# Optimization experiments

Measured on AMD Instinct MI355X. Metric: run time of the kernel, lower is better.

Reference implementation:

```python
import jax, jax.numpy as jnp
import numpy as np

B, S, D = 16, 4096, 1024
K = 65536  # number of keys == number of concepts (identity mapping)
EPS = 1e-12


def setup_inputs() -> dict:
    key = jax.random.key(0)
    k1, k2, k3, k4, k5, k6 = jax.random.split(key, 6)
    return {
        "hidden": jax.random.normal(k1, (B, S, D), dtype=jnp.float32),
        "concept_signal": jax.random.normal(k2, (B, 1, D), dtype=jnp.float32),
        "keys": jax.random.normal(k3, (K, D), dtype=jnp.float32),
        "values": jax.random.normal(k4, (K, 1, D), dtype=jnp.float32),
        "key_to_value": jnp.arange(K, dtype=jnp.int64),
        "W_layer": jax.random.normal(k5, (D, D), dtype=jnp.float32) * 0.02,
        "b_layer": jax.random.normal(k6, (D,), dtype=jnp.float32) * 0.02,
    }


def _l2norm(x, axis=-1):
    return x / jnp.maximum(jnp.linalg.norm(x, axis=axis, keepdims=True), EPS)


def reference(hidden, concept_signal, keys, values, key_to_value, W_layer, b_layer):
    # self.layer(hidden_state): Linear(D, D)
    layer_out = jnp.einsum("bsd,ed->bse", hidden, W_layer) + b_layer  # [B, S, D]

    # Tensor branch of forward: per-sample nearest-key search.
    # q: one query position per sample (P=1) -> [B, D]
    q = concept_signal[:, 0, :]
    cos = jnp.einsum("bd,kd->bk", _l2norm(q), _l2norm(keys))  # cosine similarity [B, K]
    dist = 1.0 - cos                                           # cosine distance
    chosen_key = jnp.argmin(dist, axis=1)                      # [B] nearest key per sample
    # s = 1 - smallest_dist; with threshold=-2.0 it always passes; with
    # max_tokens_per_concept=1, k = max(1, ceil(clamp(s,0,1)*1)) == 1 token.
    concept_idx = key_to_value[chosen_key]                     # [B]
    tokens = values[concept_idx, 0, :]                         # [B, D] (first of the k=1 tokens)
    tokens = _l2norm(tokens)                                   # F.normalize(..., p=2, dim=-1)
    # vstack one token onto each sample, then stack -> [B, S+1, D]
    return jnp.concatenate([layer_out, tokens[:, None, :]], axis=1)
```

## Files before the change

kernel.cpp:

```cpp
#include <hip/hip_runtime.h>

constexpr int BB = 16;
constexpr int SS = 4096;
constexpr int DD = 1024;
constexpr int KK = 65536;
constexpr int GM = BB * SS;
constexpr int GK = DD;

typedef __attribute__((ext_vector_type(8))) short bf16x8;
typedef __attribute__((ext_vector_type(4))) float f32x4;
typedef __attribute__((ext_vector_type(8))) unsigned short ushort8;

#define GLD_LDS16(g, l)                                                        \
  __builtin_amdgcn_global_load_lds(                                            \
      (const __attribute__((address_space(1))) void*)(g),                      \
      (__attribute__((address_space(3))) void*)(l), 16, 0, 0)

__device__ __forceinline__ unsigned short f2bf(float x) {
  unsigned u = __float_as_uint(x);
  u += 0x7fffu + ((u >> 16) & 1u);
  return (unsigned short)(u >> 16);
}

__device__ __forceinline__ void cvt_body(const float* __restrict__ in,
                                         unsigned short* __restrict__ out,
                                         int i) {
  const float4* p = (const float4*)in + (size_t)i * 2;
  float4 a = p[0], b = p[1];
  ushort8 r;
  r[0] = f2bf(a.x); r[1] = f2bf(a.y); r[2] = f2bf(a.z); r[3] = f2bf(a.w);
  r[4] = f2bf(b.x); r[5] = f2bf(b.y); r[6] = f2bf(b.z); r[7] = f2bf(b.w);
  *(ushort8*)(out + (size_t)i * 8) = r;
}

__global__ __launch_bounds__(256) void qsplit(const float* __restrict__ csig,
                                              unsigned short* __restrict__ qh,
                                              unsigned short* __restrict__ ql) {
  int i = blockIdx.x * 256 + threadIdx.x;
  float v = csig[i];
  unsigned short h = f2bf(v);
  float hf = __uint_as_float((unsigned)h << 16);
  qh[i] = h;
  ql[i] = f2bf(v - hf);
}

__device__ __forceinline__ void cos_mfma_body(
    const float* __restrict__ keys, const unsigned short* __restrict__ qh,
    const unsigned short* __restrict__ ql, float* __restrict__ pscore,
    int* __restrict__ pidx, int cblk, int tid,
    float (*rs)[16], int (*ri)[16]) {
  int lane = tid & 63, w = tid >> 6;
  int fr = lane & 15, kg = lane >> 4;
  int key = cblk * 64 + w * 16 + fr;

  const float* krow = keys + (size_t)key * DD + kg * 8;
  const unsigned short* qhp = qh + fr * DD + kg * 8;
  const unsigned short* qlp = ql + fr * DD + kg * 8;

  f32x4 acc = {};
  float nrm = 0.f;

  float4 ka0, kb0, ka1, kb1, ka2, kb2, ka3, kb3;
  bf16x8 h0, l0, h1, l1, h2, l2, h3, l3;

  ka0 = *(const float4*)(krow);      kb0 = *(const float4*)(krow + 4);
  h0  = *(const bf16x8*)(qhp);       l0  = *(const bf16x8*)(qlp);
  ka1 = *(const float4*)(krow + 32); kb1 = *(const float4*)(krow + 36);
  h1  = *(const bf16x8*)(qhp + 32);  l1  = *(const bf16x8*)(qlp + 32);
  ka2 = *(const float4*)(krow + 64); kb2 = *(const float4*)(krow + 68);
  h2  = *(const bf16x8*)(qhp + 64);  l2  = *(const bf16x8*)(qlp + 64);

#define COS_STEP(KA, KB, HH, LL, KAP, KBP, HP, LP, T) do {                     \
    if ((T) + 3 < 32) {                                                        \
      KAP = *(const float4*)(krow + ((T) + 3) * 32);                           \
      KBP = *(const float4*)(krow + ((T) + 3) * 32 + 4);                       \
      HP  = *(const bf16x8*)(qhp + ((T) + 3) * 32);                            \
      LP  = *(const bf16x8*)(qlp + ((T) + 3) * 32);                            \
    }                                                                          \
    float ke[8] = {KA.x, KA.y, KA.z, KA.w, KB.x, KB.y, KB.z, KB.w};            \
    ushort8 khv, klv;                                                          \
    _Pragma("unroll") for (int j = 0; j < 8; ++j) {                            \
      float v = ke[j];                                                         \
      unsigned short h = f2bf(v);                                              \
      float hf = __uint_as_float((unsigned)h << 16);                           \
      khv[j] = h;                                                              \
      klv[j] = f2bf(v - hf);                                                   \
      nrm = fmaf(v, v, nrm);                                                   \
    }                                                                          \
    bf16x8 kh8 = *(bf16x8*)&khv, kl8 = *(bf16x8*)&klv;                         \
    acc = __builtin_amdgcn_mfma_f32_16x16x32_bf16(HH, kh8, acc, 0, 0, 0);      \
    acc = __builtin_amdgcn_mfma_f32_16x16x32_bf16(LL, kh8, acc, 0, 0, 0);      \
    acc = __builtin_amdgcn_mfma_f32_16x16x32_bf16(HH, kl8, acc, 0, 0, 0);      \
  } while (0)

#pragma unroll
  for (int tt = 0; tt < 32; tt += 4) {
    COS_STEP(ka0, kb0, h0, l0, ka3, kb3, h3, l3, tt + 0);
    COS_STEP(ka1, kb1, h1, l1, ka0, kb0, h0, l0, tt + 1);
    COS_STEP(ka2, kb2, h2, l2, ka1, kb1, h1, l1, tt + 2);
    COS_STEP(ka3, kb3, h3, l3, ka2, kb2, h2, l2, tt + 3);
  }
#undef COS_STEP

  nrm += __shfl_xor(nrm, 16);
  nrm += __shfl_xor(nrm, 32);
  float inv = rsqrtf(fmaxf(nrm, 1e-24f));

#pragma unroll
  for (int j = 0; j < 4; ++j) {
    float s = acc[j] * inv;
    int i = key;
#pragma unroll
    for (int off = 1; off < 16; off <<= 1) {
      float s2 = __shfl_xor(s, off);
      int i2 = __shfl_xor(i, off);
      if (s2 > s || (s2 == s && i2 < i)) { s = s2; i = i2; }
    }
    if (fr == 0) { rs[w][kg * 4 + j] = s; ri[w][kg * 4 + j] = i; }
  }
  __syncthreads();
  if (tid < 16) {
    float bs = rs[0][tid]; int bi = ri[0][tid];
#pragma unroll
    for (int w2 = 1; w2 < 4; ++w2) {
      float s = rs[w2][tid]; int i = ri[w2][tid];
      if (s > bs || (s == bs && i < bi)) { bs = s; bi = i; }
    }
    pscore[(size_t)tid * 1024 + cblk] = bs;
    pidx[(size_t)tid * 1024 + cblk] = bi;
  }
}

__global__ __launch_bounds__(256) void fused_prep(
    const float* __restrict__ keys, const unsigned short* __restrict__ qh,
    const unsigned short* __restrict__ ql, float* __restrict__ pscore,
    int* __restrict__ pidx,
    const float* __restrict__ hidden, unsigned short* __restrict__ hbf,
    const float* __restrict__ W, unsigned short* __restrict__ wbf) {
  __shared__ float rs[4][16];
  __shared__ int ri[4][16];
  int bid = blockIdx.x, tid = threadIdx.x;
  int g = bid / 11, r = bid - g * 11;
  if (r < 2) {
    cos_mfma_body(keys, qh, ql, pscore, pidx, g * 2 + r, tid, rs, ri);
  } else {
    int v = g * 9 + (r - 2);
    if (v < 4096) {
      int base = v * 256 + tid;
#pragma unroll
      for (int q = 0; q < 8; ++q)
        cvt_body(hidden, hbf, base + q * (4096 * 256));
    } else {
      cvt_body(W, wbf, (v - 4096) * 256 + tid);
    }
  }
}


#define LDA8(AH, BUF) do {                                                     \
  _Pragma("unroll") for (int ms = 0; ms < 4; ++ms) {                           \
    int rowa = (wm << 7) + ((AH) << 6) + (ms << 4) + fr;                       \
    _Pragma("unroll") for (int ks = 0; ks < 2; ++ks) {                         \
      int ia = ((rowa << 6) + (ks << 5) + (kg << 3)) ^ sw;                     \
      ar[ms * 2 + ks] = *(const bf16x8*)&lds[(BUF) + ia]; } }                  \
} while (0)

#define LDB4(NP, BUF) do {                                                     \
  _Pragma("unroll") for (int nn = 0; nn < 2; ++nn) {                           \
    int rowb = (wn << 6) + ((((NP) << 1) + nn) << 4) + fr;                     \
    _Pragma("unroll") for (int ks = 0; ks < 2; ++ks) {                         \
      int ib = ((rowb << 6) + (ks << 5) + (kg << 3)) ^ sw;                     \
      br[(((NP) << 1) + nn) * 2 + ks] = *(const bf16x8*)&lds[(BUF) + ib]; } }  \
} while (0)

#define MFMAQ(AH, NP) do {                                                     \
  _Pragma("unroll") for (int ms = 0; ms < 4; ++ms)                             \
  _Pragma("unroll") for (int nn = 0; nn < 2; ++nn)                             \
  _Pragma("unroll") for (int ks = 0; ks < 2; ++ks)                             \
    acc[((AH) << 2) + ms][((NP) << 1) + nn] =                                  \
      __builtin_amdgcn_mfma_f32_16x16x32_bf16(ar[ms * 2 + ks],                 \
        br[(((NP) << 1) + nn) * 2 + ks],                                       \
        acc[((AH) << 2) + ms][((NP) << 1) + nn], 0, 0, 0);                     \
} while (0)

#define STAGEQ(GB, LB, QJ)                                                     \
  GLD_LDS16((GB) + (size_t)(((QJ) << 6) + srq) * GK + ssc,                     \
            &lds[(LB) + ((((QJ) << 9) + (wv << 6)) << 3)])

#define PH_MID do { __builtin_amdgcn_s_barrier();                              \
  asm volatile("s_waitcnt lgkmcnt(0)" ::: "memory");                           \
  __builtin_amdgcn_sched_barrier(0);                                           \
  __builtin_amdgcn_s_setprio(1); } while (0)

#define PH_END do { __builtin_amdgcn_s_setprio(0);                             \
  __builtin_amdgcn_s_barrier(); } while (0)

#define PH_END_V(N) do { __builtin_amdgcn_s_setprio(0);                        \
  asm volatile("s_waitcnt vmcnt(" #N ")" ::: "memory");                        \
  __builtin_amdgcn_sched_barrier(0);                                           \
  __builtin_amdgcn_s_barrier(); } while (0)

__global__ __launch_bounds__(512, 2) void gemm8(
    const unsigned short* __restrict__ A,
    const unsigned short* __restrict__ Bm,
    const float* __restrict__ bias,
    float* __restrict__ out) {
  __shared__ unsigned short lds[65536];

  int g = blockIdx.x;
  int t = ((g & 7) << 7) + (g >> 3);
  int mt = t >> 2, nt = t & 3;
  int m0 = mt << 8, n0 = nt << 8;

  int tid = threadIdx.x, lane = tid & 63, wv = tid >> 6;
  int wm = wv >> 2, wn = wv & 3;
  int fr = lane & 15, kg = lane >> 4;
  int sw = (fr & 7) << 3;

  int srq = (wv << 3) + (lane >> 3);
  int ssc = (((lane & 7) ^ ((lane >> 3) & 7)) << 3);

  const unsigned short* Ag = A + (size_t)m0 * GK;
  const unsigned short* Bg = Bm + (size_t)n0 * GK;

  f32x4 acc[8][4] = {};
  bf16x8 ar[8], br[8];

  {
    const unsigned short* b0 = Bg;
    const unsigned short* a1 = Ag + 64;
    const unsigned short* b1 = Bg + 64;
    STAGEQ(Ag, 0, 0); STAGEQ(Ag, 0, 1); STAGEQ(Ag, 0, 2); STAGEQ(Ag, 0, 3);
    STAGEQ(b0, 16384, 0); STAGEQ(b0, 16384, 1);
    STAGEQ(b0, 16384, 2); STAGEQ(b0, 16384, 3);
    STAGEQ(a1, 32768, 0); STAGEQ(a1, 32768, 2);
    STAGEQ(b1, 49152, 0); STAGEQ(b1, 49152, 1);
    STAGEQ(b1, 49152, 2); STAGEQ(b1, 49152, 3);
    asm volatile("s_waitcnt vmcnt(6)" ::: "memory");
    __builtin_amdgcn_sched_barrier(0);
    __builtin_amdgcn_s_barrier();
  }

  for (int i = 0; i < 7; ++i) {
    const unsigned short* a1 = Ag + (size_t)(2 * i + 1) * 64;
    const unsigned short* a2 = Ag + (size_t)(2 * i + 2) * 64;
    const unsigned short* b2 = Bg + (size_t)(2 * i + 2) * 64;
    const unsigned short* a3 = Ag + (size_t)(2 * i + 3) * 64;
    const unsigned short* b3 = Bg + (size_t)(2 * i + 3) * 64;
    LDA8(0, 0); LDB4(0, 16384);
    STAGEQ(a1, 32768, 1); STAGEQ(a1, 32768, 3);
    PH_MID; MFMAQ(0, 0); PH_END;
    LDB4(1, 16384);
    STAGEQ(a2, 0, 0); STAGEQ(a2, 0, 2);
    PH_MID; MFMAQ(0, 1); PH_END;
    LDA8(1, 0);
    STAGEQ(b2, 16384, 0); STAGEQ(b2, 16384, 1);
    PH_MID; MFMAQ(1, 0); PH_END;
    STAGEQ(b2, 16384, 2); STAGEQ(b2, 16384, 3);
    PH_MID; MFMAQ(1, 1); PH_END_V(6);
    LDA8(0, 32768); LDB4(0, 49152);
    STAGEQ(a2, 0, 1); STAGEQ(a2, 0, 3);
    PH_MID; MFMAQ(0, 0); PH_END;
    LDB4(1, 49152);
    STAGEQ(a3, 32768, 0); STAGEQ(a3, 32768, 2);
    PH_MID; MFMAQ(0, 1); PH_END;
    LDA8(1, 32768);
    STAGEQ(b3, 49152, 0); STAGEQ(b3, 49152, 1);
    PH_MID; MFMAQ(1, 0); PH_END;
    STAGEQ(b3, 49152, 2); STAGEQ(b3, 49152, 3);
    PH_MID; MFMAQ(1, 1); PH_END_V(6);
  }

  {
    const unsigned short* a15 = Ag + (size_t)15 * 64;
    LDA8(0, 0); LDB4(0, 16384);
    STAGEQ(a15, 32768, 1); STAGEQ(a15, 32768, 3);
    PH_MID; MFMAQ(0, 0); PH_END;
    LDB4(1, 16384); PH_MID; MFMAQ(0, 1); PH_END;
    LDA8(1, 0);     PH_MID; MFMAQ(1, 0); PH_END;
    PH_MID; MFMAQ(1, 1); PH_END_V(0);
    LDA8(0, 32768); LDB4(0, 49152); PH_MID; MFMAQ(0, 0); PH_END;
    LDB4(1, 49152); PH_MID; MFMAQ(0, 1); PH_END;
    LDA8(1, 32768); PH_MID; MFMAQ(1, 0); PH_END;
    PH_MID; MFMAQ(1, 1);
    __builtin_amdgcn_s_setprio(0);
  }

  int r0 = kg << 2, cc = fr;
#pragma unroll
  for (int ni = 0; ni < 4; ++ni) {
    int gcol = n0 + (wn << 6) + (ni << 4) + cc;
    float bv = bias[gcol];
#pragma unroll
    for (int mi = 0; mi < 8; ++mi) {
      int gr = m0 + (wm << 7) + (mi << 4) + r0;
#pragma unroll
      for (int j = 0; j < 4; ++j) {
        int grow = gr + j;
        size_t o = ((size_t)(grow + (grow >> 12)) << 10) + gcol;
        out[o] = acc[mi][ni][j] + bv;
      }
    }
  }
}

__global__ __launch_bounds__(256) void select_write(
    const float* __restrict__ pscore, const int* __restrict__ pidx, int nb,
    const int* __restrict__ ktv, const float* __restrict__ values,
    float* __restrict__ out) {
  __shared__ float ss[4];
  __shared__ int si[4];
  __shared__ float snrm;
  __shared__ int swin;
  int b = blockIdx.x, tid = threadIdx.x, lane = tid & 63, wv = tid >> 6;

  float best = -1e30f;
  int bidx = 0x7fffffff;
  for (int t = tid; t < nb; t += 256) {
    float s = pscore[(size_t)b * nb + t];
    int i = pidx[(size_t)b * nb + t];
    if (s > best || (s == best && i < bidx)) { best = s; bidx = i; }
  }
#pragma unroll
  for (int off = 32; off; off >>= 1) {
    float s = __shfl_xor(best, off);
    int i = __shfl_xor(bidx, off);
    if (s > best || (s == best && i < bidx)) { best = s; bidx = i; }
  }
  if (lane == 0) { ss[wv] = best; si[wv] = bidx; }
  __syncthreads();
  if (tid == 0) {
    float bs = ss[0]; int bi = si[0];
    for (int w2 = 1; w2 < 4; ++w2)
      if (ss[w2] > bs || (ss[w2] == bs && si[w2] < bi)) { bs = ss[w2]; bi = si[w2]; }
    swin = ktv[bi];
  }
  __syncthreads();
  int idx = swin;

  float4 v = ((const float4*)(values + (size_t)idx * DD))[tid];
  float nrm = v.x * v.x + v.y * v.y + v.z * v.z + v.w * v.w;
#pragma unroll
  for (int off = 32; off; off >>= 1) nrm += __shfl_xor(nrm, off);
  if (lane == 0) ss[wv] = nrm;
  __syncthreads();
  if (tid == 0) snrm = rsqrtf(fmaxf(ss[0] + ss[1] + ss[2] + ss[3], 1e-24f));
  __syncthreads();
  float inv = snrm;

  float4 o;
  o.x = v.x * inv; o.y = v.y * inv; o.z = v.z * inv; o.w = v.w * inv;
  ((float4*)(out + (((size_t)b * (SS + 1) + SS) << 10)))[tid] = o;
}

extern "C" void kernel_launch(void* const* d_in, const int* in_sizes, int n_in,
                              void* d_out, int out_size, void* d_ws,
                              size_t ws_size, hipStream_t stream) {
  const float* hidden = (const float*)d_in[0];
  const float* csig   = (const float*)d_in[1];
  const float* keys   = (const float*)d_in[2];
  const float* values = (const float*)d_in[3];
  const int*   ktv    = (const int*)d_in[4];
  const float* W      = (const float*)d_in[5];
  const float* bias   = (const float*)d_in[6];
  float* out = (float*)d_out;

  char* ws = (char*)d_ws;
  const size_t HB = (size_t)GM * GK * 2;
  const size_t WB = (size_t)DD * GK * 2;
  const size_t QB = (size_t)BB * DD * 2;
  const size_t PSB = (size_t)BB * 1024 * 4;

  unsigned short* hbf = (unsigned short*)ws;
  unsigned short* wbf = (unsigned short*)(ws + HB);
  unsigned short* qh  = (unsigned short*)(ws + HB + WB);
  unsigned short* ql  = (unsigned short*)(ws + HB + WB + QB);
  float* pscore = (float*)(ws + HB + WB + 2 * QB);
  int*   pidx   = (int*)(ws + HB + WB + 2 * QB + PSB);

  qsplit<<<64, 256, 0, stream>>>(csig, qh, ql);

  fused_prep<<<5632, 256, 0, stream>>>(keys, qh, ql, pscore, pidx,
                                       hidden, hbf, W, wbf);

  gemm8<<<1024, 512, 0, stream>>>(hbf, wbf, bias, out);

  select_write<<<BB, 256, 0, stream>>>(pscore, pidx, 1024, ktv, values, out);
}
```

Baseline: 374.6 us.

## Make GEMM persistent over four M tiles with cross-tile prefetch

The GEMM launch drops from 1024 to 256 blocks, and each block now loops over four consecutive 256-row M tiles that share one N tile. In the last K iteration of each tile, the first K stages of the next tile's A and the reused B are prefetched, so the pipeline does not drain and refill between tiles. This is meant to hide per-block prologue and epilogue latency and to improve B reuse. The cost is that the epilogue stores now serialize with compute inside a block, and with 256 blocks the GPU may be underfilled (about one block per CU, with launch bounds allowing two).

```diff
diff --git a/kernel.cpp b/kernel.cpp
--- a/kernel.cpp
+++ b/kernel.cpp
@@ -208,9 +208,9 @@
   __shared__ unsigned short lds[65536];
 
   int g = blockIdx.x;
-  int t = ((g & 7) << 7) + (g >> 3);
-  int mt = t >> 2, nt = t & 3;
-  int m0 = mt << 8, n0 = nt << 8;
+  int t = ((g & 7) << 5) + (g >> 3);
+  int mtb = t >> 2, nt = t & 3;
+  int n0 = nt << 8;
 
   int tid = threadIdx.x, lane = tid & 63, wv = tid >> 6;
   int wm = wv >> 2, wn = wv & 3;
@@ -220,87 +220,107 @@
   int srq = (wv << 3) + (lane >> 3);
   int ssc = (((lane & 7) ^ ((lane >> 3) & 7)) << 3);
 
-  const unsigned short* Ag = A + (size_t)m0 * GK;
   const unsigned short* Bg = Bm + (size_t)n0 * GK;
 
   f32x4 acc[8][4] = {};
   bf16x8 ar[8], br[8];
 
   {
-    const unsigned short* b0 = Bg;
+    const unsigned short* Ag = A + ((size_t)(mtb << 2) << 8) * GK;
     const unsigned short* a1 = Ag + 64;
-    const unsigned short* b1 = Bg + 64;
     STAGEQ(Ag, 0, 0); STAGEQ(Ag, 0, 1); STAGEQ(Ag, 0, 2); STAGEQ(Ag, 0, 3);
-    STAGEQ(b0, 16384, 0); STAGEQ(b0, 16384, 1);
-    STAGEQ(b0, 16384, 2); STAGEQ(b0, 16384, 3);
+    STAGEQ(Bg, 16384, 0); STAGEQ(Bg, 16384, 1);
+    STAGEQ(Bg, 16384, 2); STAGEQ(Bg, 16384, 3);
     STAGEQ(a1, 32768, 0); STAGEQ(a1, 32768, 2);
-    STAGEQ(b1, 49152, 0); STAGEQ(b1, 49152, 1);
-    STAGEQ(b1, 49152, 2); STAGEQ(b1, 49152, 3);
+    STAGEQ(Bg + 64, 49152, 0); STAGEQ(Bg + 64, 49152, 1);
+    STAGEQ(Bg + 64, 49152, 2); STAGEQ(Bg + 64, 49152, 3);
     asm volatile("s_waitcnt vmcnt(6)" ::: "memory");
     __builtin_amdgcn_sched_barrier(0);
     __builtin_amdgcn_s_barrier();
   }
 
-  for (int i = 0; i < 7; ++i) {
-    const unsigned short* a1 = Ag + (size_t)(2 * i + 1) * 64;
-    const unsigned short* a2 = Ag + (size_t)(2 * i + 2) * 64;
-    const unsigned short* b2 = Bg + (size_t)(2 * i + 2) * 64;
-    const unsigned short* a3 = Ag + (size_t)(2 * i + 3) * 64;
-    const unsigned short* b3 = Bg + (size_t)(2 * i + 3) * 64;
-    LDA8(0, 0); LDB4(0, 16384);
-    STAGEQ(a1, 32768, 1); STAGEQ(a1, 32768, 3);
-    PH_MID; MFMAQ(0, 0); PH_END;
-    LDB4(1, 16384);
-    STAGEQ(a2, 0, 0); STAGEQ(a2, 0, 2);
-    PH_MID; MFMAQ(0, 1); PH_END;
-    LDA8(1, 0);
-    STAGEQ(b2, 16384, 0); STAGEQ(b2, 16384, 1);
-    PH_MID; MFMAQ(1, 0); PH_END;
-    STAGEQ(b2, 16384, 2); STAGEQ(b2, 16384, 3);
-    PH_MID; MFMAQ(1, 1); PH_END_V(6);
-    LDA8(0, 32768); LDB4(0, 49152);
-    STAGEQ(a2, 0, 1); STAGEQ(a2, 0, 3);
-    PH_MID; MFMAQ(0, 0); PH_END;
-    LDB4(1, 49152);
-    STAGEQ(a3, 32768, 0); STAGEQ(a3, 32768, 2);
-    PH_MID; MFMAQ(0, 1); PH_END;
-    LDA8(1, 32768);
-    STAGEQ(b3, 49152, 0); STAGEQ(b3, 49152, 1);
-    PH_MID; MFMAQ(1, 0); PH_END;
-    STAGEQ(b3, 49152, 2); STAGEQ(b3, 49152, 3);
-    PH_MID; MFMAQ(1, 1); PH_END_V(6);
-  }
-
-  {
-    const unsigned short* a15 = Ag + (size_t)15 * 64;
-    LDA8(0, 0); LDB4(0, 16384);
-    STAGEQ(a15, 32768, 1); STAGEQ(a15, 32768, 3);
-    PH_MID; MFMAQ(0, 0); PH_END;
-    LDB4(1, 16384); PH_MID; MFMAQ(0, 1); PH_END;
-    LDA8(1, 0);     PH_MID; MFMAQ(1, 0); PH_END;
-    PH_MID; MFMAQ(1, 1); PH_END_V(0);
-    LDA8(0, 32768); LDB4(0, 49152); PH_MID; MFMAQ(0, 0); PH_END;
-    LDB4(1, 49152); PH_MID; MFMAQ(0, 1); PH_END;
-    LDA8(1, 32768); PH_MID; MFMAQ(1, 0); PH_END;
-    PH_MID; MFMAQ(1, 1);
-    __builtin_amdgcn_s_setprio(0);
-  }
-
-  int r0 = kg << 2, cc = fr;
-#pragma unroll
-  for (int ni = 0; ni < 4; ++ni) {
-    int gcol = n0 + (wn << 6) + (ni << 4) + cc;
-    float bv = bias[gcol];
-#pragma unroll
-    for (int mi = 0; mi < 8; ++mi) {
-      int gr = m0 + (wm << 7) + (mi << 4) + r0;
-#pragma unroll
-      for (int j = 0; j < 4; ++j) {
-        int grow = gr + j;
-        size_t o = ((size_t)(grow + (grow >> 12)) << 10) + gcol;
-        out[o] = acc[mi][ni][j] + bv;
+  for (int tv = 0; tv < 4; ++tv) {
+    int m0 = ((mtb << 2) + tv) << 8;
+    const unsigned short* Ag = A + (size_t)m0 * GK;
+    const unsigned short* nAg = A + (size_t)(m0 + (tv < 3 ? 256 : 0)) * GK;
+
+    for (int i = 0; i < 7; ++i) {
+      const unsigned short* a1 = Ag + (size_t)(2 * i + 1) * 64;
+      const unsigned short* a2 = Ag + (size_t)(2 * i + 2) * 64;
+      const unsigned short* b2 = Bg + (size_t)(2 * i + 2) * 64;
+      const unsigned short* a3 = Ag + (size_t)(2 * i + 3) * 64;
+      const unsigned short* b3 = Bg + (size_t)(2 * i + 3) * 64;
+      LDA8(0, 0); LDB4(0, 16384);
+      STAGEQ(a1, 32768, 1); STAGEQ(a1, 32768, 3);
+      PH_MID; MFMAQ(0, 0); PH_END;
+      LDB4(1, 16384);
+      STAGEQ(a2, 0, 0); STAGEQ(a2, 0, 2);
+      PH_MID; MFMAQ(0, 1); PH_END;
+      LDA8(1, 0);
+      STAGEQ(b2, 16384, 0); STAGEQ(b2, 16384, 1);
+      PH_MID; MFMAQ(1, 0); PH_END;
+      STAGEQ(b2, 16384, 2); STAGEQ(b2, 16384, 3);
+      PH_MID; MFMAQ(1, 1); PH_END_V(6);
+      LDA8(0, 32768); LDB4(0, 49152);
+      STAGEQ(a2, 0, 1); STAGEQ(a2, 0, 3);
+      PH_MID; MFMAQ(0, 0); PH_END;
+      LDB4(1, 49152);
+      STAGEQ(a3, 32768, 0); STAGEQ(a3, 32768, 2);
+      PH_MID; MFMAQ(0, 1); PH_END;
+      LDA8(1, 32768);
+      STAGEQ(b3, 49152, 0); STAGEQ(b3, 49152, 1);
+      PH_MID; MFMAQ(1, 0); PH_END;
+      STAGEQ(b3, 49152, 2); STAGEQ(b3, 49152, 3);
+      PH_MID; MFMAQ(1, 1); PH_END_V(6);
+    }
+
+    {
+      const unsigned short* a15 = Ag + (size_t)15 * 64;
+      LDA8(0, 0); LDB4(0, 16384);
+      STAGEQ(a15, 32768, 1); STAGEQ(a15, 32768, 3);
+      PH_MID; MFMAQ(0, 0); PH_END;
+      LDB4(1, 16384);
+      STAGEQ(nAg, 0, 0); STAGEQ(nAg, 0, 2);
+      PH_MID; MFMAQ(0, 1); PH_END;
+      LDA8(1, 0);
+      STAGEQ(Bg, 16384, 0); STAGEQ(Bg, 16384, 1);
+      PH_MID; MFMAQ(1, 0); PH_END;
+      STAGEQ(nAg, 0, 1); STAGEQ(nAg, 0, 3);
+      PH_MID; MFMAQ(1, 1); PH_END_V(6);
+      LDA8(0, 32768); LDB4(0, 49152);
+      STAGEQ(Bg, 16384, 2); STAGEQ(Bg, 16384, 3);
+      PH_MID; MFMAQ(0, 0); PH_END;
+      LDB4(1, 49152);
+      STAGEQ(nAg + 64, 32768, 0); STAGEQ(nAg + 64, 32768, 2);
+      PH_MID; MFMAQ(0, 1); PH_END;
+      LDA8(1, 32768);
+      STAGEQ(Bg + 64, 49152, 0); STAGEQ(Bg + 64, 49152, 1);
+      PH_MID; MFMAQ(1, 0); PH_END;
+      STAGEQ(Bg + 64, 49152, 2); STAGEQ(Bg + 64, 49152, 3);
+      PH_MID; MFMAQ(1, 1); PH_END_V(6);
+    }
+
+    int r0 = kg << 2, cc = fr;
+#pragma unroll
+    for (int ni = 0; ni < 4; ++ni) {
+      int gcol = n0 + (wn << 6) + (ni << 4) + cc;
+      float bv = bias[gcol];
+#pragma unroll
+      for (int mi = 0; mi < 8; ++mi) {
+        int gr = m0 + (wm << 7) + (mi << 4) + r0;
+#pragma unroll
+        for (int j = 0; j < 4; ++j) {
+          int grow = gr + j;
+          size_t o = ((size_t)(grow + (grow >> 12)) << 10) + gcol;
+          out[o] = acc[mi][ni][j] + bv;
+        }
       }
     }
+#pragma unroll
+    for (int mi = 0; mi < 8; ++mi)
+#pragma unroll
+      for (int ni = 0; ni < 4; ++ni)
+        acc[mi][ni] = (f32x4){0.f, 0.f, 0.f, 0.f};
   }
 }
 
@@ -383,7 +403,7 @@
   fused_prep<<<5632, 256, 0, stream>>>(keys, qh, ql, pscore, pidx,
                                        hidden, hbf, W, wbf);
 
-  gemm8<<<1024, 512, 0, stream>>>(hbf, wbf, bias, out);
+  gemm8<<<256, 512, 0, stream>>>(hbf, wbf, bias, out);
 
   select_write<<<BB, 256, 0, stream>>>(pscore, pidx, 1024, ktv, values, out);
 }
```

New measurement: 542.1 us. 44.7% more time.

## Split cosine search across four D-chunks and add a combine kernel

Applied to the files above, without the earlier changes.

The key-query dot product is now split along the feature dimension into four chunks of 256. Each fused_prep cosine block handles one chunk and writes partial dot products and partial norms to a workspace, instead of doing a full 1024-wide reduction per block. A new cos_combine kernel sums the partials, normalizes, and does the argmax reduction. This adds parallelism and interleaving with the conversion work, at the cost of about 17 MB of extra partial-result traffic and one more kernel launch.

```diff
diff --git a/kernel.cpp b/kernel.cpp
--- a/kernel.cpp
+++ b/kernel.cpp
@@ -46,16 +46,17 @@
 
 __device__ __forceinline__ void cos_mfma_body(
     const float* __restrict__ keys, const unsigned short* __restrict__ qh,
-    const unsigned short* __restrict__ ql, float* __restrict__ pscore,
-    int* __restrict__ pidx, int cblk, int tid,
-    float (*rs)[16], int (*ri)[16]) {
+    const unsigned short* __restrict__ ql, float* __restrict__ pd,
+    float* __restrict__ pn, int cblk, int tid) {
   int lane = tid & 63, w = tid >> 6;
   int fr = lane & 15, kg = lane >> 4;
-  int key = cblk * 64 + w * 16 + fr;
-
-  const float* krow = keys + (size_t)key * DD + kg * 8;
-  const unsigned short* qhp = qh + fr * DD + kg * 8;
-  const unsigned short* qlp = ql + fr * DD + kg * 8;
+  int dc = cblk >> 10, kgrp = cblk & 1023;
+  int key = kgrp * 64 + w * 16 + fr;
+  int d0 = dc << 8;
+
+  const float* krow = keys + (size_t)key * DD + d0 + kg * 8;
+  const unsigned short* qhp = qh + fr * DD + d0 + kg * 8;
+  const unsigned short* qlp = ql + fr * DD + d0 + kg * 8;
 
   f32x4 acc = {};
   float nrm = 0.f;
@@ -71,7 +72,7 @@
   h2  = *(const bf16x8*)(qhp + 64);  l2  = *(const bf16x8*)(qlp + 64);
 
 #define COS_STEP(KA, KB, HH, LL, KAP, KBP, HP, LP, T) do {                     \
-    if ((T) + 3 < 32) {                                                        \
+    if ((T) + 3 < 8) {                                                         \
       KAP = *(const float4*)(krow + ((T) + 3) * 32);                           \
       KBP = *(const float4*)(krow + ((T) + 3) * 32 + 4);                       \
       HP  = *(const bf16x8*)(qhp + ((T) + 3) * 32);                            \
@@ -94,7 +95,7 @@
   } while (0)
 
 #pragma unroll
-  for (int tt = 0; tt < 32; tt += 4) {
+  for (int tt = 0; tt < 8; tt += 4) {
     COS_STEP(ka0, kb0, h0, l0, ka3, kb3, h3, l3, tt + 0);
     COS_STEP(ka1, kb1, h1, l1, ka0, kb0, h0, l0, tt + 1);
     COS_STEP(ka2, kb2, h2, l2, ka1, kb1, h1, l1, tt + 2);
@@ -104,47 +105,24 @@
 
   nrm += __shfl_xor(nrm, 16);
   nrm += __shfl_xor(nrm, 32);
-  float inv = rsqrtf(fmaxf(nrm, 1e-24f));
-
-#pragma unroll
-  for (int j = 0; j < 4; ++j) {
-    float s = acc[j] * inv;
-    int i = key;
-#pragma unroll
-    for (int off = 1; off < 16; off <<= 1) {
-      float s2 = __shfl_xor(s, off);
-      int i2 = __shfl_xor(i, off);
-      if (s2 > s || (s2 == s && i2 < i)) { s = s2; i = i2; }
-    }
-    if (fr == 0) { rs[w][kg * 4 + j] = s; ri[w][kg * 4 + j] = i; }
-  }
-  __syncthreads();
-  if (tid < 16) {
-    float bs = rs[0][tid]; int bi = ri[0][tid];
-#pragma unroll
-    for (int w2 = 1; w2 < 4; ++w2) {
-      float s = rs[w2][tid]; int i = ri[w2][tid];
-      if (s > bs || (s == bs && i < bi)) { bs = s; bi = i; }
-    }
-    pscore[(size_t)tid * 1024 + cblk] = bs;
-    pidx[(size_t)tid * 1024 + cblk] = bi;
-  }
+
+  *(float4*)(pd + ((size_t)dc * KK + key) * 16 + kg * 4) =
+      make_float4(acc[0], acc[1], acc[2], acc[3]);
+  if (kg == 0) pn[(size_t)dc * KK + key] = nrm;
 }
 
 __global__ __launch_bounds__(256) void fused_prep(
     const float* __restrict__ keys, const unsigned short* __restrict__ qh,
-    const unsigned short* __restrict__ ql, float* __restrict__ pscore,
-    int* __restrict__ pidx,
+    const unsigned short* __restrict__ ql, float* __restrict__ pd,
+    float* __restrict__ pn,
     const float* __restrict__ hidden, unsigned short* __restrict__ hbf,
     const float* __restrict__ W, unsigned short* __restrict__ wbf) {
-  __shared__ float rs[4][16];
-  __shared__ int ri[4][16];
   int bid = blockIdx.x, tid = threadIdx.x;
-  int g = bid / 11, r = bid - g * 11;
-  if (r < 2) {
-    cos_mfma_body(keys, qh, ql, pscore, pidx, g * 2 + r, tid, rs, ri);
+  int g = bid / 17, r = bid - g * 17;
+  if (r < 8) {
+    cos_mfma_body(keys, qh, ql, pd, pn, g * 8 + r, tid);
   } else {
-    int v = g * 9 + (r - 2);
+    int v = g * 9 + (r - 8);
     if (v < 4096) {
       int base = v * 256 + tid;
 #pragma unroll
@@ -153,6 +131,55 @@
     } else {
       cvt_body(W, wbf, (v - 4096) * 256 + tid);
     }
+  }
+}
+
+__global__ __launch_bounds__(256) void cos_combine(
+    const float* __restrict__ pd, const float* __restrict__ pn,
+    float* __restrict__ pscore, int* __restrict__ pidx) {
+  __shared__ float rs[4][16];
+  __shared__ int ri[4][16];
+  int tid = threadIdx.x, lane = tid & 63, w = tid >> 6;
+  int k = blockIdx.x * 256 + tid;
+
+  float d[16] = {0.f, 0.f, 0.f, 0.f, 0.f, 0.f, 0.f, 0.f,
+                 0.f, 0.f, 0.f, 0.f, 0.f, 0.f, 0.f, 0.f};
+  float nrm = 0.f;
+#pragma unroll
+  for (int dc = 0; dc < 4; ++dc) {
+    const float4* p = (const float4*)(pd + ((size_t)dc * KK + k) * 16);
+#pragma unroll
+    for (int i = 0; i < 4; ++i) {
+      float4 v = p[i];
+      d[i * 4 + 0] += v.x; d[i * 4 + 1] += v.y;
+      d[i * 4 + 2] += v.z; d[i * 4 + 3] += v.w;
+    }
+    nrm += pn[(size_t)dc * KK + k];
+  }
+  float inv = rsqrtf(fmaxf(nrm, 1e-24f));
+
+#pragma unroll
+  for (int b = 0; b < 16; ++b) {
+    float s = d[b] * inv;
+    int i = k;
+#pragma unroll
+    for (int off = 32; off; off >>= 1) {
+      float s2 = __shfl_xor(s, off);
+      int i2 = __shfl_xor(i, off);
+      if (s2 > s || (s2 == s && i2 < i)) { s = s2; i = i2; }
+    }
+    if (lane == 0) { rs[w][b] = s; ri[w][b] = i; }
+  }
+  __syncthreads();
+  if (tid < 16) {
+    float bs = rs[0][tid]; int bi = ri[0][tid];
+#pragma unroll
+    for (int w2 = 1; w2 < 4; ++w2) {
+      float s = rs[w2][tid]; int i = ri[w2][tid];
+      if (s > bs || (s == bs && i < bi)) { bs = s; bi = i; }
+    }
+    pscore[(size_t)tid * gridDim.x + blockIdx.x] = bs;
+    pidx[(size_t)tid * gridDim.x + blockIdx.x] = bi;
   }
 }
 
@@ -366,24 +393,30 @@
   float* out = (float*)d_out;
 
   char* ws = (char*)d_ws;
-  const size_t HB = (size_t)GM * GK * 2;
-  const size_t WB = (size_t)DD * GK * 2;
-  const size_t QB = (size_t)BB * DD * 2;
-  const size_t PSB = (size_t)BB * 1024 * 4;
+  const size_t HB  = (size_t)GM * GK * 2;
+  const size_t WB  = (size_t)DD * GK * 2;
+  const size_t QB  = (size_t)BB * DD * 2;
+  const size_t PDB = (size_t)4 * KK * 16 * 4;
+  const size_t PNB = (size_t)4 * KK * 4;
+  const size_t PSB = (size_t)BB * 256 * 4;
 
   unsigned short* hbf = (unsigned short*)ws;
   unsigned short* wbf = (unsigned short*)(ws + HB);
   unsigned short* qh  = (unsigned short*)(ws + HB + WB);
   unsigned short* ql  = (unsigned short*)(ws + HB + WB + QB);
-  float* pscore = (float*)(ws + HB + WB + 2 * QB);
-  int*   pidx   = (int*)(ws + HB + WB + 2 * QB + PSB);
+  float* pd     = (float*)(ws + HB + WB + 2 * QB);
+  float* pn     = (float*)(ws + HB + WB + 2 * QB + PDB);
+  float* pscore = (float*)(ws + HB + WB + 2 * QB + PDB + PNB);
+  int*   pidx   = (int*)(ws + HB + WB + 2 * QB + PDB + PNB + PSB);
 
   qsplit<<<64, 256, 0, stream>>>(csig, qh, ql);
 
-  fused_prep<<<5632, 256, 0, stream>>>(keys, qh, ql, pscore, pidx,
+  fused_prep<<<8704, 256, 0, stream>>>(keys, qh, ql, pd, pn,
                                        hidden, hbf, W, wbf);
 
+  cos_combine<<<256, 256, 0, stream>>>(pd, pn, pscore, pidx);
+
   gemm8<<<1024, 512, 0, stream>>>(hbf, wbf, bias, out);
 
-  select_write<<<BB, 256, 0, stream>>>(pscore, pidx, 1024, ktv, values, out);
-}
+  select_write<<<BB, 256, 0, stream>>>(pscore, pidx, 256, ktv, values, out);
+}
```

New measurement: 385.3 us. +2.8%, slower.
